# Optimization experiments

Hardware: AMD Instinct MI355X
Metric: run time of the kernel (lower is better)

The kernel has to match this reference:

```python
import jax, jax.numpy as jnp
import numpy as np

EMBED_DIM = 512
NUM_HEADS = 8
HEAD_DIM = EMBED_DIM // NUM_HEADS  # 64


def setup_inputs() -> dict:
    key = jax.random.key(0)
    ks = jax.random.split(key, 9)
    B, N, E, H, D = 4, 1024, EMBED_DIM, NUM_HEADS, HEAD_DIM
    s = 1.0 / np.sqrt(E)  # ~ nn.Linear init scale
    x = jax.random.normal(ks[0], (B, N, E), dtype=jnp.float32)
    # weights stored as (in, out): y = x @ W + b (same math as torch x @ W.T)
    Wq = jax.random.uniform(ks[1], (E, E), jnp.float32, -s, s)
    bq = jax.random.uniform(ks[2], (E,), jnp.float32, -s, s)
    Wk = jax.random.uniform(ks[3], (E, E), jnp.float32, -s, s)
    bk = jax.random.uniform(ks[4], (E,), jnp.float32, -s, s)
    Wv = jax.random.uniform(ks[5], (E, E), jnp.float32, -s, s)
    bv = jax.random.uniform(ks[6], (E,), jnp.float32, -s, s)
    Wg = jax.random.uniform(ks[7], (E, H * D * D), jnp.float32, -s, s)
    bg = jax.random.uniform(ks[8], (H * D * D,), jnp.float32, -s, s)
    return {"x": x, "Wq": Wq, "bq": bq, "Wk": Wk, "bk": bk,
            "Wv": Wv, "bv": bv, "Wg": Wg, "bg": bg}


def reference(x, Wq, bq, Wk, bk, Wv, bv, Wg, bg):
    B, N, E = x.shape
    H, D = NUM_HEADS, HEAD_DIM
    # per-token generated transform g: [B, N, H, D, D] (act = exact GELU)
    g = jax.nn.gelu(x @ Wg + bg, approximate=False).reshape(B, N, H, D, D)
    q = (x @ Wq + bq).reshape(B, N, H, D)
    k = (x @ Wk + bk).reshape(B, N, H, D)
    v = (x @ Wv + bv).reshape(B, N, H, D)
    # q' = q @ g  (per-token, per-head 1xD @ DxD)
    qg = jnp.einsum("bnhd,bnhde->bnhe", q, g)
    # attention scores (note: no 1/sqrt(d) scaling in the original)
    att = jnp.einsum("bnhe,bmhe->bhnm", qg, k)
    att = jax.nn.softmax(att, axis=-1)
    out = jnp.einsum("bhnm,bmhd->bnhd", att, v)
    return out.reshape(B, N, E)
```

## Files before the change

### kernel.cpp

```cpp
#include <hip/hip_runtime.h>
#include <math.h>

#define TOK   4096
#define EDIM  512
#define HEADS 8
#define DHEAD 64
#define GCOLS 32768

typedef unsigned short u16;
typedef _Float16 f16;
typedef __attribute__((ext_vector_type(8))) f16 f16x8;
typedef __attribute__((ext_vector_type(4))) f16 f16x4;
typedef __attribute__((ext_vector_type(4))) float f32x4;
typedef __attribute__((ext_vector_type(4))) unsigned short u16x4;
typedef __attribute__((ext_vector_type(8))) unsigned short u16x8;

typedef const __attribute__((address_space(1))) void* gas_ptr;
typedef __attribute__((address_space(3))) void* las_ptr;

__device__ __forceinline__ void gll16(const void* g, void* lds) {
  __builtin_amdgcn_global_load_lds((gas_ptr)g, (las_ptr)lds, 16, 0, 0);
}

#define WAITV(N) asm volatile("s_waitcnt vmcnt(" #N ")" ::: "memory")
__device__ __forceinline__ void barrier_raw() { asm volatile("s_barrier" ::: "memory"); }

__device__ __forceinline__ u16 f2h_bits(float f) {
  union { f16 h; u16 u; } v; v.h = (f16)f;
  return v.u;
}

__device__ __forceinline__ float fast_gelu(float x) {
  float s = x * 0.7071067811865475f;
  float ax = fabsf(s);
  float t = __builtin_amdgcn_rcpf(1.0f + 0.3275911f * ax);
  float poly = t * (0.254829592f + t * (-0.284496736f + t * (1.421413741f +
               t * (-1.453152027f + t * 1.061405429f))));
  float e = __expf(-ax * ax);
  float r = 1.0f - poly * e;
  float erfv = copysignf(r, s);
  return 0.5f * x * (1.0f + erfv);
}

__global__ void cast_f16_k(const float* __restrict__ in, u16* __restrict__ out, int n) {
  int i = (blockIdx.x * blockDim.x + threadIdx.x) * 4;
  if (i + 3 < n) {
    float4 f = *(const float4*)(in + i);
    u16x4 h;
    h.x = f2h_bits(f.x); h.y = f2h_bits(f.y);
    h.z = f2h_bits(f.z); h.w = f2h_bits(f.w);
    *(u16x4*)(out + i) = h;
  }
}

__global__ void transpose_f16_wide_k(const float* __restrict__ in, u16* __restrict__ out,
                                     int K, int N) {
  __shared__ float tile[64][65];
  const int n0 = blockIdx.x * 64, k0 = blockIdx.y * 64;
  const int tid = threadIdx.x;
  #pragma unroll
  for (int i = 0; i < 4; i++) {
    int c = tid + i * 256;
    int kr = c >> 4, c4 = (c & 15) * 4;
    float4 f = *(const float4*)(in + (size_t)(k0 + kr) * N + n0 + c4);
    tile[kr][c4 + 0] = f.x;
    tile[kr][c4 + 1] = f.y;
    tile[kr][c4 + 2] = f.z;
    tile[kr][c4 + 3] = f.w;
  }
  __syncthreads();
  #pragma unroll
  for (int i = 0; i < 2; i++) {
    int c = tid + i * 256;
    int nr = c >> 3, kc = (c & 7) * 8;
    u16x8 h;
    #pragma unroll
    for (int e = 0; e < 8; e++)
      h[e] = f2h_bits(tile[kc + e][nr]);
    *(u16x8*)(out + (size_t)(n0 + nr) * K + k0 + kc) = h;
  }
}

__global__ void transpose3_f16_k(const float* __restrict__ Wq, const float* __restrict__ Wk,
                                 const float* __restrict__ Wv, u16* __restrict__ Wqt,
                                 u16* __restrict__ Wkt, u16* __restrict__ Wvt) {
  __shared__ float tile[64][65];
  const int which = blockIdx.z;
  const float* in = which == 0 ? Wq : (which == 1 ? Wk : Wv);
  u16* out = which == 0 ? Wqt : (which == 1 ? Wkt : Wvt);
  const int n0 = blockIdx.x * 64, k0 = blockIdx.y * 64;
  const int tid = threadIdx.x;
  #pragma unroll
  for (int i = 0; i < 4; i++) {
    int c = tid + i * 256;
    int kr = c >> 4, c4 = (c & 15) * 4;
    float4 f = *(const float4*)(in + (size_t)(k0 + kr) * EDIM + n0 + c4);
    tile[kr][c4 + 0] = f.x;
    tile[kr][c4 + 1] = f.y;
    tile[kr][c4 + 2] = f.z;
    tile[kr][c4 + 3] = f.w;
  }
  __syncthreads();
  #pragma unroll
  for (int i = 0; i < 2; i++) {
    int c = tid + i * 256;
    int nr = c >> 3, kc = (c & 7) * 8;
    u16x8 h;
    #pragma unroll
    for (int e = 0; e < 8; e++)
      h[e] = f2h_bits(tile[kc + e][nr]);
    *(u16x8*)(out + (size_t)(n0 + nr) * EDIM + k0 + kc) = h;
  }
}

__global__ __launch_bounds__(256, 2) void qkv_gemm_k(
    const u16* __restrict__ xf, const u16* __restrict__ Wqt,
    const u16* __restrict__ Wkt, const u16* __restrict__ Wvt,
    const float* __restrict__ bq, const float* __restrict__ bk, const float* __restrict__ bv,
    u16* __restrict__ qho, u16* __restrict__ ko, u16* __restrict__ vTo) {
  __shared__ __align__(16) u16 As[2][16 * 512];
  __shared__ __align__(16) u16 Bs[2][16 * 512];
  const int which = blockIdx.z;
  const u16* Wt = which == 0 ? Wqt : (which == 1 ? Wkt : Wvt);
  const float* bias = which == 0 ? bq : (which == 1 ? bk : bv);
  const int m0 = blockIdx.x * 128;
  const int n0 = blockIdx.y * 128;
  const int tid = threadIdx.x;
  const int w = tid >> 6, lane = tid & 63, l15 = lane & 15, quad = lane >> 4;
  const int mhalf = w >> 1, nhalf = w & 1;

  f32x4 acc[4][4];
  #pragma unroll
  for (int i = 0; i < 4; i++)
    #pragma unroll
    for (int j = 0; j < 4; j++) acc[i][j] = f32x4{0.f, 0.f, 0.f, 0.f};

  auto stage = [&](int d, int kk) {
    #pragma unroll
    for (int i = 0; i < 8; i++) {
      int cb = w * 8 + i;
      if (cb < 16) {
        int ks = cb >> 3, mt = cb & 7;
        gll16(xf + (size_t)(m0 + mt * 16 + l15) * 512 + kk + ks * 32 + quad * 8,
              As[d] + cb * 512);
      } else {
        int bi = cb - 16, ks = bi >> 3, nt = bi & 7;
        gll16(Wt + (size_t)(n0 + nt * 16 + l15) * 512 + kk + ks * 32 + quad * 8,
              Bs[d] + bi * 512);
      }
    }
  };

  stage(0, 0);
  int cur = 0;
  for (int kt = 0; kt < 8; kt++) {
    if (kt < 7) { stage(cur ^ 1, (kt + 1) * 64); WAITV(8); }
    else        { WAITV(0); }
    barrier_raw();
    const u16* Asb = As[cur];
    const u16* Bsb = Bs[cur];
    #pragma unroll
    for (int ks = 0; ks < 2; ks++) {
      f16x8 a[4], b[4];
      #pragma unroll
      for (int mt = 0; mt < 4; mt++)
        a[mt] = *(const f16x8*)(Asb + (ks * 8 + mhalf * 4 + mt) * 512 + lane * 8);
      #pragma unroll
      for (int nt = 0; nt < 4; nt++)
        b[nt] = *(const f16x8*)(Bsb + (ks * 8 + nhalf * 4 + nt) * 512 + lane * 8);
      #pragma unroll
      for (int mt = 0; mt < 4; mt++)
        #pragma unroll
        for (int nt = 0; nt < 4; nt++)
          acc[mt][nt] = __builtin_amdgcn_mfma_f32_16x16x32_f16(a[mt], b[nt], acc[mt][nt], 0, 0, 0);
    }
    barrier_raw();
    cur ^= 1;
  }
  #pragma unroll
  for (int nt = 0; nt < 4; nt++) {
    int col = n0 + (nhalf * 4 + nt) * 16 + l15;
    float bia = bias[col];
    int h = col >> 6, d = col & 63;
    #pragma unroll
    for (int mt = 0; mt < 4; mt++) {
      #pragma unroll
      for (int r = 0; r < 4; r++) {
        int t = m0 + (mhalf * 4 + mt) * 16 + quad * 4 + r;
        int b_ = t >> 10, n = t & 1023;
        float val = acc[mt][nt][r] + bia;
        size_t idx = (((size_t)(b_ * 8 + h) * 1024) + n) * 64 + d;
        if (which == 0)      qho[idx] = f2h_bits(val);
        else if (which == 1) ko[idx] = f2h_bits(val);
        else                 vTo[(((size_t)(b_ * 8 + h) * 64) + d) * 1024 + n] = f2h_bits(val);
      }
    }
  }
}

__global__ __launch_bounds__(512, 2) void qg_fused_k(
    const u16* __restrict__ xf, const u16* __restrict__ Wgt,
    const float* __restrict__ bg, const u16* __restrict__ qh,
    u16* __restrict__ qg16) {
  __shared__ __align__(16) u16 As[2][16 * 512];
  __shared__ __align__(16) u16 Bs[2][32 * 512];
  __shared__ __align__(16) u16 Qs[128 * 64];
  __shared__ __align__(16) float bgs[4096];
  const int head = blockIdx.x & 7;
  const int t0 = (blockIdx.x >> 3) * 128;
  const int tid = threadIdx.x;
  const int w = tid >> 6, lane = tid & 63, l15 = lane & 15, quad = lane >> 4;
  const int mhalf = w >> 2;
  const int ntA = w & 3;
  const int b_ = t0 >> 10, nseq0 = t0 & 1023;
  const u16* qbase = qh + (((size_t)(b_ * 8 + head) * 1024) + nseq0) * 64;
  const float* bgbase = bg + head * 4096;

  #pragma unroll
  for (int i = 0; i < 2; i++) {
    int cb = w * 2 + i;
    gll16(qbase + (size_t)cb * 512 + (size_t)lane * 8, Qs + (size_t)cb * 512);
    gll16(bgbase + (size_t)cb * 256 + (size_t)lane * 4, bgs + (size_t)cb * 256);
  }

  auto stage = [&](int d, int s) {
    int jp = s >> 3, kk = (s & 7) << 6;
    int c0 = head * 4096 + jp * 256;
    #pragma unroll
    for (int i = 0; i < 6; i++) {
      int cb = w * 6 + i;
      if (cb < 16) {
        int ks = cb >> 3, mt = cb & 7;
        gll16(xf + (size_t)(t0 + mt * 16 + l15) * 512 + kk + ks * 32 + quad * 8,
              As[d] + cb * 512);
      } else {
        int bi = cb - 16, ks = bi >> 4, nt = bi & 15;
        gll16(Wgt + (size_t)(c0 + nt * 16 + l15) * 512 + kk + ks * 32 + quad * 8,
              Bs[d] + bi * 512);
      }
    }
  };

  f32x4 qg[4];
  #pragma unroll
  for (int i = 0; i < 4; i++) qg[i] = f32x4{0.f, 0.f, 0.f, 0.f};
  f32x4 zacc[4][4];
  #pragma unroll
  for (int i = 0; i < 4; i++)
    #pragma unroll
    for (int z = 0; z < 4; z++) zacc[i][z] = f32x4{0.f, 0.f, 0.f, 0.f};

  stage(0, 0);
  int cur = 0;
  for (int s = 0; s < 128; s++) {
    if (s < 127) { stage(cur ^ 1, s + 1); WAITV(6); }
    else         { WAITV(0); }
    barrier_raw();
    const u16* Asb = As[cur];
    const u16* Bsb = Bs[cur];
    #pragma unroll
    for (int ks = 0; ks < 2; ks++) {
      f16x8 a[4];
      #pragma unroll
      for (int mt = 0; mt < 4; mt++)
        a[mt] = *(const f16x8*)(Asb + (ks * 8 + mhalf * 4 + mt) * 512 + lane * 8);
      #pragma unroll
      for (int z = 0; z < 4; z++) {
        int nt = (z >> 1) * 8 + (z & 1) * 4 + ntA;
        f16x8 b = *(const f16x8*)(Bsb + (ks * 16 + nt) * 512 + lane * 8);
        #pragma unroll
        for (int mt = 0; mt < 4; mt++)
          zacc[mt][z] = __builtin_amdgcn_mfma_f32_16x16x32_f16(a[mt], b, zacc[mt][z], 0, 0, 0);
      }
    }
    if ((s & 7) == 7) {
      int jp = s >> 3;
      float bgv[4];
      #pragma unroll
      for (int z = 0; z < 4; z++) {
        int nt = (z >> 1) * 8 + (z & 1) * 4 + ntA;
        bgv[z] = bgs[jp * 256 + nt * 16 + l15];
      }
      const int d0 = 4 * jp;
      #pragma unroll
      for (int mt = 0; mt < 4; mt++) {
        #pragma unroll
        for (int r = 0; r < 4; r++) {
          int row = mhalf * 64 + mt * 16 + quad * 4 + r;
          f16x4 qp = *(const f16x4*)(Qs + row * 64 + d0);
          float g0 = fast_gelu(zacc[mt][0][r] + bgv[0]);
          float g1 = fast_gelu(zacc[mt][1][r] + bgv[1]);
          float g2 = fast_gelu(zacc[mt][2][r] + bgv[2]);
          float g3 = fast_gelu(zacc[mt][3][r] + bgv[3]);
          qg[mt][r] += (float)qp.x * g0 + (float)qp.y * g1 +
                       (float)qp.z * g2 + (float)qp.w * g3;
        }
      }
      #pragma unroll
      for (int i = 0; i < 4; i++)
        #pragma unroll
        for (int z = 0; z < 4; z++) zacc[i][z] = f32x4{0.f, 0.f, 0.f, 0.f};
    }
    barrier_raw();
    cur ^= 1;
  }
  const int eb = ntA * 16;
  #pragma unroll
  for (int mt = 0; mt < 4; mt++) {
    #pragma unroll
    for (int r = 0; r < 4; r++) {
      int t = t0 + mhalf * 64 + mt * 16 + quad * 4 + r;
      int bb = t >> 10, n = t & 1023;
      qg16[(((size_t)(bb * 8 + head) * 1024) + n) * 64 + eb + l15] = f2h_bits(qg[mt][r]);
    }
  }
}

__global__ __launch_bounds__(256, 2) void attn_k(
    const u16* __restrict__ qg16, const u16* __restrict__ kb,
    const u16* __restrict__ vTb, float* __restrict__ out) {
  __shared__ __align__(16) u16 Ks[2][8 * 512];
  __shared__ __align__(16) u16 Vs[2][8 * 512];
  __shared__ __align__(16) f16 Ps[4][16 * 72];
  const int idx = blockIdx.x;
  const int bh = idx & 31;
  const int qt = idx >> 5;
  const int b_ = bh >> 3, h = bh & 7;
  const int tid = threadIdx.x;
  const int w = tid >> 6, lane = tid & 63, l15 = lane & 15, quad = lane >> 4;

  const u16* qgB = qg16 + (size_t)bh * 1024 * 64;
  const u16* kB  = kb  + (size_t)bh * 1024 * 64;
  const u16* vB  = vTb + (size_t)bh * 64 * 1024;

  f16x8 aq[2];
  #pragma unroll
  for (int ks = 0; ks < 2; ks++)
    aq[ks] = *(const f16x8*)(qgB + (size_t)(qt * 64 + w * 16 + l15) * 64 + ks * 32 + quad * 8);

  f32x4 o[4];
  #pragma unroll
  for (int i = 0; i < 4; i++) o[i] = f32x4{0.f, 0.f, 0.f, 0.f};
  float m_old[4], l_old[4];
  #pragma unroll
  for (int r = 0; r < 4; r++) { m_old[r] = -1e30f; l_old[r] = 0.f; }

  auto stageKV = [&](int d, int kt) {
    #pragma unroll
    for (int i = 0; i < 2; i++) {
      int cb = w * 2 + i;
      int ks = cb >> 2, nt = cb & 3;
      gll16(kB + (size_t)(kt * 64 + nt * 16 + l15) * 64 + ks * 32 + quad * 8, Ks[d] + cb * 512);
      gll16(vB + (size_t)(nt * 16 + l15) * 1024 + kt * 64 + ks * 32 + quad * 8, Vs[d] + cb * 512);
    }
  };

  stageKV(0, 0);
  int cur = 0;
  for (int kt = 0; kt < 16; kt++) {
    if (kt < 15) { stageKV(cur ^ 1, kt + 1); WAITV(4); }
    else         { WAITV(0); }
    barrier_raw();
    f32x4 s[4];
    #pragma unroll
    for (int nt = 0; nt < 4; nt++) s[nt] = f32x4{0.f, 0.f, 0.f, 0.f};
    #pragma unroll
    for (int ks = 0; ks < 2; ks++)
      #pragma unroll
      for (int nt = 0; nt < 4; nt++) {
        f16x8 kf = *(const f16x8*)(Ks[cur] + (ks * 4 + nt) * 512 + lane * 8);
        s[nt] = __builtin_amdgcn_mfma_f32_16x16x32_f16(aq[ks], kf, s[nt], 0, 0, 0);
      }
    float rmax[4];
    #pragma unroll
    for (int r = 0; r < 4; r++)
      rmax[r] = fmaxf(fmaxf(s[0][r], s[1][r]), fmaxf(s[2][r], s[3][r]));
    #pragma unroll
    for (int off = 1; off < 16; off <<= 1)
      #pragma unroll
      for (int r = 0; r < 4; r++)
        rmax[r] = fmaxf(rmax[r], __shfl_xor(rmax[r], off));
    float alpha[4], rsum[4];
    #pragma unroll
    for (int r = 0; r < 4; r++) {
      float mn = fmaxf(m_old[r], rmax[r]);
      alpha[r] = __expf(m_old[r] - mn);
      m_old[r] = mn;
      rsum[r] = 0.f;
    }
    #pragma unroll
    for (int nt = 0; nt < 4; nt++)
      #pragma unroll
      for (int r = 0; r < 4; r++) {
        float p = __expf(s[nt][r] - m_old[r]);
        rsum[r] += p;
        Ps[w][(quad * 4 + r) * 72 + nt * 16 + l15] = (f16)p;
      }
    #pragma unroll
    for (int off = 1; off < 16; off <<= 1)
      #pragma unroll
      for (int r = 0; r < 4; r++)
        rsum[r] += __shfl_xor(rsum[r], off);
    #pragma unroll
    for (int r = 0; r < 4; r++) l_old[r] = l_old[r] * alpha[r] + rsum[r];
    #pragma unroll
    for (int nt = 0; nt < 4; nt++)
      #pragma unroll
      for (int r = 0; r < 4; r++) o[nt][r] *= alpha[r];
    #pragma unroll
    for (int ks = 0; ks < 2; ks++) {
      f16x8 pa = *(const f16x8*)(&Ps[w][l15 * 72 + ks * 32 + quad * 8]);
      #pragma unroll
      for (int nt = 0; nt < 4; nt++) {
        f16x8 vf = *(const f16x8*)(Vs[cur] + (ks * 4 + nt) * 512 + lane * 8);
        o[nt] = __builtin_amdgcn_mfma_f32_16x16x32_f16(pa, vf, o[nt], 0, 0, 0);
      }
    }
    barrier_raw();
    cur ^= 1;
  }
  #pragma unroll
  for (int r = 0; r < 4; r++) {
    float inv = 1.f / l_old[r];
    int n = qt * 64 + w * 16 + quad * 4 + r;
    #pragma unroll
    for (int nt = 0; nt < 4; nt++)
      out[((size_t)(b_ * 1024 + n)) * 512 + h * 64 + nt * 16 + l15] = o[nt][r] * inv;
  }
}

extern "C" void kernel_launch(void* const* d_in, const int* in_sizes, int n_in,
                              void* d_out, int out_size, void* d_ws, size_t ws_size,
                              hipStream_t stream) {
  const float* x  = (const float*)d_in[0];
  const float* Wq = (const float*)d_in[1];
  const float* bq = (const float*)d_in[2];
  const float* Wk = (const float*)d_in[3];
  const float* bk = (const float*)d_in[4];
  const float* Wv = (const float*)d_in[5];
  const float* bv = (const float*)d_in[6];
  const float* Wg = (const float*)d_in[7];
  const float* bg = (const float*)d_in[8];
  float* out = (float*)d_out;

  const size_t NX = (size_t)TOK * EDIM;
  const size_t NWG = (size_t)GCOLS * EDIM;
  const size_t NW = (size_t)EDIM * EDIM;

  char* p = (char*)d_ws;
  u16* xf  = (u16*)p; p += NX * 2;
  u16* Wgt = (u16*)p; p += NWG * 2;
  u16* Wqt = (u16*)p; p += NW * 2;
  u16* Wkt = (u16*)p; p += NW * 2;
  u16* Wvt = (u16*)p; p += NW * 2;
  u16* qh  = (u16*)p; p += NX * 2;
  u16* kf  = (u16*)p; p += NX * 2;
  u16* vT  = (u16*)p; p += NX * 2;
  u16* qg16 = (u16*)p; p += NX * 2;

  hipLaunchKernelGGL(cast_f16_k, dim3(NX / 1024), dim3(256), 0, stream,
                     x, xf, (int)NX);
  hipLaunchKernelGGL(transpose3_f16_k, dim3(EDIM / 64, EDIM / 64, 3), dim3(256), 0, stream,
                     Wq, Wk, Wv, Wqt, Wkt, Wvt);
  hipLaunchKernelGGL(transpose_f16_wide_k, dim3(GCOLS / 64, EDIM / 64), dim3(256), 0, stream,
                     Wg, Wgt, EDIM, GCOLS);
  hipLaunchKernelGGL(qkv_gemm_k, dim3(TOK / 128, EDIM / 128, 3), dim3(256), 0, stream,
                     xf, Wqt, Wkt, Wvt, bq, bk, bv, qh, kf, vT);
  hipLaunchKernelGGL(qg_fused_k, dim3(256), dim3(512), 0, stream,
                     xf, Wgt, bg, qh, qg16);
  hipLaunchKernelGGL(attn_k, dim3(512), dim3(256), 0, stream,
                     qg16, kf, vT, out);
}
```

Before: 422.5 us.

## Retile qg fused GEMM to 256-token blocks with split-D partial sums

The fused Wg GEMM + GELU + q·g kernel now uses 1024-thread blocks covering 256 tokens, and splits each head's 64 d-rows into two halves handled by different blocks. That doubles x-tile reuse per Wg tile and halves the loop length per block. Each half writes fp32 partial qg results, and the attention kernel sums the two partials and converts to fp16 when loading q. The cost is extra workspace, fp32 partial writes and reads, and lower occupancy from one large block per CU.

```diff
diff --git a/kernel.cpp b/kernel.cpp
--- a/kernel.cpp
+++ b/kernel.cpp
@@ -198,46 +198,44 @@
   }
 }
 
-__global__ __launch_bounds__(512, 2) void qg_fused_k(
+__global__ __launch_bounds__(1024, 1) void qg_fused_k(
     const u16* __restrict__ xf, const u16* __restrict__ Wgt,
     const float* __restrict__ bg, const u16* __restrict__ qh,
-    u16* __restrict__ qg16) {
-  __shared__ __align__(16) u16 As[2][16 * 512];
+    float* __restrict__ qgp) {
+  __shared__ __align__(16) u16 As[2][32 * 512];
   __shared__ __align__(16) u16 Bs[2][32 * 512];
-  __shared__ __align__(16) u16 Qs[128 * 64];
-  __shared__ __align__(16) float bgs[4096];
+  __shared__ __align__(16) u16 Qs[256 * 32];
+  __shared__ __align__(16) float bgs[2048];
   const int head = blockIdx.x & 7;
-  const int t0 = (blockIdx.x >> 3) * 128;
+  const int jh = (blockIdx.x >> 3) & 1;
+  const int t0 = (blockIdx.x >> 4) * 256;
   const int tid = threadIdx.x;
   const int w = tid >> 6, lane = tid & 63, l15 = lane & 15, quad = lane >> 4;
-  const int mhalf = w >> 2;
+  const int mq = w >> 2;
   const int ntA = w & 3;
   const int b_ = t0 >> 10, nseq0 = t0 & 1023;
-  const u16* qbase = qh + (((size_t)(b_ * 8 + head) * 1024) + nseq0) * 64;
-  const float* bgbase = bg + head * 4096;
-
-  #pragma unroll
-  for (int i = 0; i < 2; i++) {
-    int cb = w * 2 + i;
-    gll16(qbase + (size_t)cb * 512 + (size_t)lane * 8, Qs + (size_t)cb * 512);
-    gll16(bgbase + (size_t)cb * 256 + (size_t)lane * 4, bgs + (size_t)cb * 256);
-  }
+  const int bh = b_ * 8 + head;
+  const u16* qbase = qh + (((size_t)bh * 1024) + nseq0) * 64;
+  const float* bgbase = bg + head * 4096 + jh * 2048;
+
+  gll16(qbase + (size_t)(w * 16 + (lane >> 2)) * 64 + jh * 32 + (lane & 3) * 8,
+        Qs + w * 512);
+  gll16(bgbase + (size_t)(w & 7) * 256 + (size_t)lane * 4, bgs + (w & 7) * 256);
 
   auto stage = [&](int d, int s) {
     int jp = s >> 3, kk = (s & 7) << 6;
-    int c0 = head * 4096 + jp * 256;
-    #pragma unroll
-    for (int i = 0; i < 6; i++) {
-      int cb = w * 6 + i;
-      if (cb < 16) {
-        int ks = cb >> 3, mt = cb & 7;
-        gll16(xf + (size_t)(t0 + mt * 16 + l15) * 512 + kk + ks * 32 + quad * 8,
-              As[d] + cb * 512);
-      } else {
-        int bi = cb - 16, ks = bi >> 4, nt = bi & 15;
-        gll16(Wgt + (size_t)(c0 + nt * 16 + l15) * 512 + kk + ks * 32 + quad * 8,
-              Bs[d] + bi * 512);
-      }
+    const u16* bsrc = Wgt + (size_t)(head * 4096 + jh * 2048 + jp * 256) * 512;
+    #pragma unroll
+    for (int i = 0; i < 2; i++) {
+      int cb = w * 2 + i, ks = cb >> 4, mt = cb & 15;
+      gll16(xf + (size_t)(t0 + mt * 16 + l15) * 512 + kk + ks * 32 + quad * 8,
+            As[d] + cb * 512);
+    }
+    #pragma unroll
+    for (int i = 0; i < 2; i++) {
+      int bi = w * 2 + i, ks = bi >> 4, nt = bi & 15;
+      gll16(bsrc + (size_t)(nt * 16 + l15) * 512 + kk + ks * 32 + quad * 8,
+            Bs[d] + bi * 512);
     }
   };
 
@@ -252,9 +250,9 @@
 
   stage(0, 0);
   int cur = 0;
-  for (int s = 0; s < 128; s++) {
-    if (s < 127) { stage(cur ^ 1, s + 1); WAITV(6); }
-    else         { WAITV(0); }
+  for (int s = 0; s < 64; s++) {
+    if (s < 63) { stage(cur ^ 1, s + 1); WAITV(4); }
+    else        { WAITV(0); }
     barrier_raw();
     const u16* Asb = As[cur];
     const u16* Bsb = Bs[cur];
@@ -263,7 +261,7 @@
       f16x8 a[4];
       #pragma unroll
       for (int mt = 0; mt < 4; mt++)
-        a[mt] = *(const f16x8*)(Asb + (ks * 8 + mhalf * 4 + mt) * 512 + lane * 8);
+        a[mt] = *(const f16x8*)(Asb + (ks * 16 + mq * 4 + mt) * 512 + lane * 8);
       #pragma unroll
       for (int z = 0; z < 4; z++) {
         int nt = (z >> 1) * 8 + (z & 1) * 4 + ntA;
@@ -281,13 +279,13 @@
         int nt = (z >> 1) * 8 + (z & 1) * 4 + ntA;
         bgv[z] = bgs[jp * 256 + nt * 16 + l15];
       }
-      const int d0 = 4 * jp;
+      const int d0 = jp * 4;
       #pragma unroll
       for (int mt = 0; mt < 4; mt++) {
         #pragma unroll
         for (int r = 0; r < 4; r++) {
-          int row = mhalf * 64 + mt * 16 + quad * 4 + r;
-          f16x4 qp = *(const f16x4*)(Qs + row * 64 + d0);
+          int row = mq * 64 + mt * 16 + quad * 4 + r;
+          f16x4 qp = *(const f16x4*)(Qs + row * 32 + d0);
           float g0 = fast_gelu(zacc[mt][0][r] + bgv[0]);
           float g1 = fast_gelu(zacc[mt][1][r] + bgv[1]);
           float g2 = fast_gelu(zacc[mt][2][r] + bgv[2]);
@@ -304,20 +302,21 @@
     barrier_raw();
     cur ^= 1;
   }
+  float* outp = qgp + (size_t)jh * TOK * 512 + ((size_t)bh * 1024) * 64;
   const int eb = ntA * 16;
   #pragma unroll
   for (int mt = 0; mt < 4; mt++) {
     #pragma unroll
     for (int r = 0; r < 4; r++) {
-      int t = t0 + mhalf * 64 + mt * 16 + quad * 4 + r;
-      int bb = t >> 10, n = t & 1023;
-      qg16[(((size_t)(bb * 8 + head) * 1024) + n) * 64 + eb + l15] = f2h_bits(qg[mt][r]);
+      int tok = mq * 64 + mt * 16 + quad * 4 + r;
+      int n = nseq0 + tok;
+      outp[(size_t)n * 64 + eb + l15] = qg[mt][r];
     }
   }
 }
 
 __global__ __launch_bounds__(256, 2) void attn_k(
-    const u16* __restrict__ qg16, const u16* __restrict__ kb,
+    const float* __restrict__ qgp, const u16* __restrict__ kb,
     const u16* __restrict__ vTb, float* __restrict__ out) {
   __shared__ __align__(16) u16 Ks[2][8 * 512];
   __shared__ __align__(16) u16 Vs[2][8 * 512];
@@ -329,14 +328,21 @@
   const int tid = threadIdx.x;
   const int w = tid >> 6, lane = tid & 63, l15 = lane & 15, quad = lane >> 4;
 
-  const u16* qgB = qg16 + (size_t)bh * 1024 * 64;
+  const float* qg0 = qgp + ((size_t)bh * 1024) * 64;
+  const float* qg1 = qg0 + (size_t)TOK * 512;
   const u16* kB  = kb  + (size_t)bh * 1024 * 64;
   const u16* vB  = vTb + (size_t)bh * 64 * 1024;
 
   f16x8 aq[2];
   #pragma unroll
-  for (int ks = 0; ks < 2; ks++)
-    aq[ks] = *(const f16x8*)(qgB + (size_t)(qt * 64 + w * 16 + l15) * 64 + ks * 32 + quad * 8);
+  for (int ks = 0; ks < 2; ks++) {
+    size_t off = (size_t)(qt * 64 + w * 16 + l15) * 64 + ks * 32 + quad * 8;
+    f16x8 v;
+    #pragma unroll
+    for (int e = 0; e < 8; e++)
+      v[e] = (f16)(qg0[off + e] + qg1[off + e]);
+    aq[ks] = v;
+  }
 
   f32x4 o[4];
   #pragma unroll
@@ -456,7 +462,7 @@
   u16* qh  = (u16*)p; p += NX * 2;
   u16* kf  = (u16*)p; p += NX * 2;
   u16* vT  = (u16*)p; p += NX * 2;
-  u16* qg16 = (u16*)p; p += NX * 2;
+  float* qgp = (float*)p; p += NX * 4 * 2;
 
   hipLaunchKernelGGL(cast_f16_k, dim3(NX / 1024), dim3(256), 0, stream,
                      x, xf, (int)NX);
@@ -466,8 +472,8 @@
                      Wg, Wgt, EDIM, GCOLS);
   hipLaunchKernelGGL(qkv_gemm_k, dim3(TOK / 128, EDIM / 128, 3), dim3(256), 0, stream,
                      xf, Wqt, Wkt, Wvt, bq, bk, bv, qh, kf, vT);
-  hipLaunchKernelGGL(qg_fused_k, dim3(256), dim3(512), 0, stream,
-                     xf, Wgt, bg, qh, qg16);
+  hipLaunchKernelGGL(qg_fused_k, dim3(256), dim3(1024), 0, stream,
+                     xf, Wgt, bg, qh, qgp);
   hipLaunchKernelGGL(attn_k, dim3(512), dim3(256), 0, stream,
-                     qg16, kf, vT, out);
-}
+                     qgp, kf, vT, out);
+}
```

Result: no change. 428.3 us (+1.4%).
